# Kernel optimization log

Hardware: AMD Instinct MI355X
Metric: run time of the kernel (lower is better)

Reference implementation:

```python
import jax, jax.numpy as jnp
import numpy as np

N, C, T, H, W = 2, 512, 8, 28, 28
THW = T * H * W
BN_EPS = 1e-5


def conv1x1(x, Wt, b):
    # pointwise channel mixing, equivalent to 1x1 Conv2d/Conv3d on (N,C,T,H,W)
    return jnp.einsum('oc,ncthw->nothw', Wt, x) + b[None, :, None, None, None]


def setup_inputs() -> dict:
    key = jax.random.key(0)
    ks = jax.random.split(key, 8)
    s = 1.0 / np.sqrt(C)
    x = jax.random.normal(ks[0], (N, C, T, H, W), dtype=jnp.float32)
    mask = jax.random.uniform(ks[1], (N, C, T, H, W), dtype=jnp.float32)
    Wh = jax.random.normal(ks[2], (C, C), dtype=jnp.float32) * s
    Wg = jax.random.normal(ks[3], (C, C), dtype=jnp.float32) * s
    Wm = jax.random.normal(ks[4], (C, C), dtype=jnp.float32) * s
    Wz = jax.random.normal(ks[5], (C, C), dtype=jnp.float32) * s  # kaiming-like
    bh = jnp.zeros((C,), jnp.float32)
    bg = jnp.zeros((C,), jnp.float32)
    bm = jnp.zeros((C,), jnp.float32)
    bz = jnp.zeros((C,), jnp.float32)
    bn_w = jnp.ones((C,), jnp.float32)
    bn_b = jnp.zeros((C,), jnp.float32)
    gamma = jnp.float32(1.0)  # self.gamma (undefined in source __init__); learnable scalar
    return dict(x=x, mask=mask, Wh=Wh, bh=bh, Wg=Wg, bg=bg, Wm=Wm, bm=bm,
                Wz=Wz, bz=bz, bn_w=bn_w, bn_b=bn_b, gamma=gamma)


def reference(x, mask, Wh, bh, Wg, bg, Wm, bm, Wz, bz, bn_w, bn_b, gamma):
    n = x.shape[0]
    # proj_f = h(x) reshaped (N, THW, C); proj_g = g(x) (N, C, THW)
    ph_x = conv1x1(x, Wh, bh).reshape(n, C, THW)
    pg = conv1x1(x, Wg, bg).reshape(n, C, THW)
    # energy[n,t,s] = sum_c ph_x[n,c,t] * pg[n,c,s]  -> (N, THW, THW)
    energy = jnp.einsum('nct,ncs->nts', ph_x, pg)
    attention = jax.nn.softmax(energy, axis=-1)
    # proj_h uses self.h on mask (faithful to source)
    ph_m = conv1x1(mask, Wh, bh).reshape(n, C, THW)
    # bmm(proj_h, attention^T): [n,c,t] = sum_s ph_m[n,c,s] * attention[n,t,s]
    mask_energy = jnp.einsum('ncs,nts->nct', ph_m, attention)
    mask_atten = jax.nn.softmax(mask_energy, axis=-1)  # softmax over THW
    pm = conv1x1(x, Wm, bm)
    out = pm * mask_atten.reshape(n, C, T, H, W)
    # W_z: 1x1 Conv3d + BatchNorm3d (training-mode batch stats, weight=1, bias=0)
    wy = conv1x1(x, Wz, bz)
    mu = jnp.mean(wy, axis=(0, 2, 3, 4), keepdims=True)
    var = jnp.var(wy, axis=(0, 2, 3, 4), keepdims=True)
    wy = (wy - mu) * jax.lax.rsqrt(var + BN_EPS)
    wy = wy * bn_w[None, :, None, None, None] + bn_b[None, :, None, None, None]
    return gamma * out + wy
```

## Files before the change

kernel.cpp:

```cpp
#include <hip/hip_runtime.h>
#include <hip/hip_bf16.h>
#include <math.h>

#define NN 2
#define CC 512
#define PP 6272
#define TCHMAX 1664
#define NCHK 4
#define NJT 49
#define KSP 4
#define EM 64.0f
static const size_t PPC = (size_t)PP * CC;
static const size_t NCP = (size_t)NN * PPC;

typedef unsigned short ushortT;
typedef __attribute__((ext_vector_type(8))) short short8;
typedef __attribute__((ext_vector_type(4))) float f32x4;

__device__ __forceinline__ ushortT f2bf(float f) {
  __hip_bfloat16 h = __float2bfloat16(f);
  return *reinterpret_cast<ushortT*>(&h);
}
__device__ __forceinline__ float bf2f(ushortT u) {
  return __uint_as_float(((unsigned)u) << 16);
}

__device__ __forceinline__ void ld_g2l(const void* g, void* l) {
  __builtin_amdgcn_global_load_lds(
      (const __attribute__((address_space(1))) void*)g,
      (__attribute__((address_space(3))) void*)l, 16, 0, 0);
}

__global__ __launch_bounds__(256) void k_cast4(const float* __restrict__ W0,
                                               const float* __restrict__ W1,
                                               const float* __restrict__ W2,
                                               const float* __restrict__ W3,
                                               ushortT* __restrict__ dst) {
  const float* src = (blockIdx.y == 0) ? W0 : (blockIdx.y == 1) ? W1
                    : (blockIdx.y == 2) ? W2 : W3;
  const int i = (blockIdx.x * 256 + threadIdx.x) * 4;
  float4 v = *(const float4*)&src[i];
  ushort4 o;
  o.x = f2bf(v.x); o.y = f2bf(v.y); o.z = f2bf(v.z); o.w = f2bf(v.w);
  *(ushort4*)&dst[(size_t)blockIdx.y * CC * CC + i] = o;
}

__global__ void k_castT(const float* __restrict__ in, ushortT* __restrict__ out) {
  __shared__ float T[32][33];
  const int p0 = blockIdx.x * 32, c0 = blockIdx.y * 32;
  const int tx = threadIdx.x, ty = threadIdx.y;
  const size_t nbi = (size_t)blockIdx.z * PPC;
#pragma unroll
  for (int i = 0; i < 4; ++i)
    T[ty + i * 8][tx] = in[nbi + (size_t)(c0 + ty + i * 8) * PP + p0 + tx];
  __syncthreads();
#pragma unroll
  for (int i = 0; i < 4; ++i) {
    int r = ty + i * 8;
    out[nbi + (size_t)(p0 + r) * CC + c0 + tx] = f2bf(T[tx][r]);
  }
}

template <int OM>
__global__ __launch_bounds__(256) void k_bgemm(const ushortT* __restrict__ A,
                                               const ushortT* __restrict__ B,
                                               const float* __restrict__ bias,
                                               ushortT* __restrict__ out,
                                               int KD, size_t sAn, size_t sBn,
                                               size_t sOn, int ldo) {
  __shared__ __align__(16) ushortT smem[17408];
  ushortT* At = smem;
  ushortT* Bt = smem + 8192;
  const int tid = threadIdx.x;
  const int l = tid & 63, w = tid >> 6;
  const int j0 = blockIdx.x * 128;
  const int i0 = blockIdx.y * 128;
  A += (size_t)blockIdx.z * sAn;
  B += (size_t)blockIdx.z * sBn;
  out += (size_t)blockIdx.z * sOn;
  const int wi = (w & 1) * 64, wj = (w >> 1) * 64;
  const int lr = l & 15, lk = l >> 4;
  const int sr = l >> 3, scg = l & 7;

  f32x4 acc[4][4] = {};

  for (int k0 = 0; k0 < KD; k0 += 64) {
#pragma unroll
    for (int i = 0; i < 4; ++i) {
      int row = w * 32 + i * 8 + sr;
      int cs = scg ^ (row & 7);
      ld_g2l(A + (size_t)(i0 + row) * KD + k0 + cs * 8, (char*)At + (w * 4 + i) * 1024);
      ld_g2l(B + (size_t)(j0 + row) * KD + k0 + cs * 8, (char*)Bt + (w * 4 + i) * 1024);
    }
    __syncthreads();
#pragma unroll
    for (int ks = 0; ks < 2; ++ks) {
      short8 af[4], bfv[4];
      const int cc = ks * 4 + lk;
#pragma unroll
      for (int tt = 0; tt < 4; ++tt) {
        int row = wi + tt * 16 + lr;
        af[tt] = *(const short8*)((const char*)At + row * 128 + ((cc ^ (row & 7)) * 16));
      }
#pragma unroll
      for (int ss = 0; ss < 4; ++ss) {
        int row = wj + ss * 16 + lr;
        bfv[ss] = *(const short8*)((const char*)Bt + row * 128 + ((cc ^ (row & 7)) * 16));
      }
#pragma unroll
      for (int tt = 0; tt < 4; ++tt)
#pragma unroll
        for (int ss = 0; ss < 4; ++ss)
          acc[tt][ss] = __builtin_amdgcn_mfma_f32_16x16x32_bf16(af[tt], bfv[ss], acc[tt][ss], 0, 0, 0);
    }
    __syncthreads();
  }
  const int r4 = (l >> 4) * 4;
  ushortT (*Tr)[136] = (ushortT(*)[136])smem;
  if (OM == 0) {
    float bj[4];
#pragma unroll
    for (int ss = 0; ss < 4; ++ss) bj[ss] = bias[j0 + wj + ss * 16 + lr];
#pragma unroll
    for (int tt = 0; tt < 4; ++tt)
#pragma unroll
      for (int r = 0; r < 4; ++r) {
        int row = wi + tt * 16 + r4 + r;
#pragma unroll
        for (int ss = 0; ss < 4; ++ss)
          Tr[row][wj + ss * 16 + lr] = f2bf(acc[tt][ss][r] + bj[ss]);
      }
  } else {
#pragma unroll
    for (int tt = 0; tt < 4; ++tt)
#pragma unroll
      for (int r = 0; r < 4; ++r) {
        int row = wi + tt * 16 + r4 + r;
        float bi = bias[i0 + row];
#pragma unroll
        for (int ss = 0; ss < 4; ++ss)
          Tr[row][wj + ss * 16 + lr] = f2bf(acc[tt][ss][r] + bi);
      }
  }
  __syncthreads();
#pragma unroll
  for (int q = 0; q < 8; ++q) {
    int chunk = q * 256 + tid;
    int row = chunk >> 4, cg = chunk & 15;
    short8 v = *(const short8*)&Tr[row][cg * 8];
    *(short8*)&out[(size_t)(i0 + row) * ldo + j0 + cg * 8] = v;
  }
}

__global__ __launch_bounds__(256) void k_energy(const ushortT* __restrict__ phxT,
                                                const ushortT* __restrict__ pgT,
                                                ushortT* __restrict__ Ech,
                                                float* __restrict__ Estat,
                                                int tbase) {
  __shared__ __align__(16) ushortT smem[17408];
  __shared__ float Ss[128][2];
  ushortT* At = smem;
  ushortT* Bt = smem + 8192;
  const int tid = threadIdx.x;
  const int l = tid & 63, w = tid >> 6;
  const int j0 = blockIdx.x * 128;
  const int i0 = blockIdx.y * 128;
  const int z = blockIdx.z;
  const ushortT* A = phxT + (size_t)z * PPC + (size_t)tbase * CC;
  const ushortT* B = pgT + (size_t)z * PPC;
  ushortT* out = Ech + (size_t)z * TCHMAX * PP;
  const int wi = (w & 1) * 64, wj = (w >> 1) * 64;
  const int lr = l & 15, lk = l >> 4;
  const int sr = l >> 3, scg = l & 7;

  f32x4 acc[4][4] = {};

  for (int k0 = 0; k0 < CC; k0 += 64) {
#pragma unroll
    for (int i = 0; i < 4; ++i) {
      int row = w * 32 + i * 8 + sr;
      int cs = scg ^ (row & 7);
      ld_g2l(A + (size_t)(i0 + row) * CC + k0 + cs * 8, (char*)At + (w * 4 + i) * 1024);
      ld_g2l(B + (size_t)(j0 + row) * CC + k0 + cs * 8, (char*)Bt + (w * 4 + i) * 1024);
    }
    __syncthreads();
#pragma unroll
    for (int ks = 0; ks < 2; ++ks) {
      short8 af[4], bfv[4];
      const int cc = ks * 4 + lk;
#pragma unroll
      for (int tt = 0; tt < 4; ++tt) {
        int row = wi + tt * 16 + lr;
        af[tt] = *(const short8*)((const char*)At + row * 128 + ((cc ^ (row & 7)) * 16));
      }
#pragma unroll
      for (int ss = 0; ss < 4; ++ss) {
        int row = wj + ss * 16 + lr;
        bfv[ss] = *(const short8*)((const char*)Bt + row * 128 + ((cc ^ (row & 7)) * 16));
      }
#pragma unroll
      for (int tt = 0; tt < 4; ++tt)
#pragma unroll
        for (int ss = 0; ss < 4; ++ss)
          acc[tt][ss] = __builtin_amdgcn_mfma_f32_16x16x32_bf16(af[tt], bfv[ss], acc[tt][ss], 0, 0, 0);
    }
    __syncthreads();
  }
  const int r4 = (l >> 4) * 4;
  const int jh = w >> 1;
  ushortT (*Tr)[136] = (ushortT(*)[136])smem;
#pragma unroll
  for (int tt = 0; tt < 4; ++tt)
#pragma unroll
    for (int r = 0; r < 4; ++r) {
      int row = wi + tt * 16 + r4 + r;
      float u0 = __expf(acc[tt][0][r] - EM);
      float u1 = __expf(acc[tt][1][r] - EM);
      float u2 = __expf(acc[tt][2][r] - EM);
      float u3 = __expf(acc[tt][3][r] - EM);
      Tr[row][wj + lr]      = f2bf(u0);
      Tr[row][wj + 16 + lr] = f2bf(u1);
      Tr[row][wj + 32 + lr] = f2bf(u2);
      Tr[row][wj + 48 + lr] = f2bf(u3);
      float sx = (u0 + u1) + (u2 + u3);
#pragma unroll
      for (int d = 1; d < 16; d <<= 1) sx += __shfl_xor(sx, d);
      if (lr == 0) Ss[row][jh] = sx;
    }
  __syncthreads();
  if (tid < 128) {
    Estat[((size_t)z * TCHMAX + i0 + tid) * NJT + blockIdx.x] =
        Ss[tid][0] + Ss[tid][1];
  }
#pragma unroll
  for (int q = 0; q < 8; ++q) {
    int chunk = q * 256 + tid;
    int row = chunk >> 4, cg = chunk & 15;
    short8 v = *(const short8*)&Tr[row][cg * 8];
    *(short8*)&out[(size_t)(i0 + row) * PP + j0 + cg * 8] = v;
  }
}

__global__ __launch_bounds__(256) void k_zcomb(const float* __restrict__ Estat,
                                               float* __restrict__ rowZ, int rows) {
  const int r = blockIdx.x * 256 + threadIdx.x;
  if (r >= NN * rows) return;
  const int z = r / rows, tl = r % rows;
  const float* p = Estat + ((size_t)z * TCHMAX + tl) * NJT;
  float s = 0.f;
#pragma unroll
  for (int j = 0; j < NJT; ++j) s += p[j];
  rowZ[z * TCHMAX + tl] = 1.0f / s;
}

__global__ __launch_bounds__(256) void k_me(const ushortT* __restrict__ phmB,
                                            const ushortT* __restrict__ Ech,
                                            ushortT* __restrict__ mePart) {
  __shared__ __align__(16) ushortT smem[12288];
  ushortT* At = smem;
  ushortT* Bt = smem + 8192;
  const int tid = threadIdx.x;
  const int l = tid & 63, w = tid >> 6;
  const int tl0 = blockIdx.x * 64;
  const int c0 = blockIdx.y * 128;
  const int bz = blockIdx.z;
  const int z = bz / KSP, ks = bz % KSP;
  const size_t nb = (size_t)z * PPC;
  const ushortT* Pb = Ech + (size_t)z * TCHMAX * PP;
  const int wc = (w & 1) * 64, wt = (w >> 1) * 32;
  const int lr = l & 15, lk = l >> 4;
  const int sr = l >> 3, scg = l & 7;

  f32x4 acc[4][2] = {};

  const int sBeg = ((ks * 98) / KSP) * 64;
  const int sEnd = (((ks + 1) * 98) / KSP) * 64;
  for (int s0 = sBeg; s0 < sEnd; s0 += 64) {
#pragma unroll
    for (int i = 0; i < 4; ++i) {
      int row = w * 32 + i * 8 + sr;
      int cs = scg ^ (row & 7);
      ld_g2l(phmB + nb + (size_t)(c0 + row) * PP + s0 + cs * 8,
             (char*)At + (w * 4 + i) * 1024);
    }
#pragma unroll
    for (int i = 0; i < 2; ++i) {
      int row = w * 16 + i * 8 + sr;
      int cs = scg ^ (row & 7);
      ld_g2l(Pb + (size_t)(tl0 + row) * PP + s0 + cs * 8,
             (char*)Bt + (w * 2 + i) * 1024);
    }
    __syncthreads();
#pragma unroll
    for (int kk = 0; kk < 2; ++kk) {
      short8 af[4], bfv[2];
      const int cc = kk * 4 + lk;
#pragma unroll
      for (int ct = 0; ct < 4; ++ct) {
        int row = wc + ct * 16 + lr;
        af[ct] = *(const short8*)((const char*)At + row * 128 + ((cc ^ (row & 7)) * 16));
      }
#pragma unroll
      for (int tt = 0; tt < 2; ++tt) {
        int row = wt + tt * 16 + lr;
        bfv[tt] = *(const short8*)((const char*)Bt + row * 128 + ((cc ^ (row & 7)) * 16));
      }
#pragma unroll
      for (int ct = 0; ct < 4; ++ct)
#pragma unroll
        for (int tt = 0; tt < 2; ++tt)
          acc[ct][tt] = __builtin_amdgcn_mfma_f32_16x16x32_bf16(af[ct], bfv[tt], acc[ct][tt], 0, 0, 0);
    }
    __syncthreads();
  }
  const int r4 = (l >> 4) * 4;
  ushortT (*Tr)[72] = (ushortT(*)[72])smem;
#pragma unroll
  for (int ct = 0; ct < 4; ++ct)
#pragma unroll
    for (int r = 0; r < 4; ++r) {
      int row = wc + ct * 16 + r4 + r;
#pragma unroll
      for (int tt = 0; tt < 2; ++tt)
        Tr[row][wt + tt * 16 + lr] = f2bf(acc[ct][tt][r]);
    }
  __syncthreads();
  ushortT* out = mePart + ((size_t)(ks * NN + z) * CC) * TCHMAX;
#pragma unroll
  for (int q = 0; q < 4; ++q) {
    int chunk = q * 256 + tid;
    int row = chunk >> 3, cg = chunk & 7;
    short8 v = *(const short8*)&Tr[row][cg * 8];
    *(short8*)&out[(size_t)(c0 + row) * TCHMAX + tl0 + cg * 8] = v;
  }
}

__global__ __launch_bounds__(256) void k_meadd(const ushortT* __restrict__ mePart,
                                               const float* __restrict__ rowZ,
                                               ushortT* __restrict__ meb,
                                               int tbase, int rows) {
  const int idx = (blockIdx.x * 256 + threadIdx.x) * 4;
  const int tl = idx % rows;
  const int c = (idx / rows) % CC;
  const int z = idx / (rows * CC);
  float s0 = 0.f, s1 = 0.f, s2 = 0.f, s3 = 0.f;
#pragma unroll
  for (int ks = 0; ks < KSP; ++ks) {
    const size_t o = ((size_t)(ks * NN + z) * CC + c) * TCHMAX + tl;
    ushort4 a = *(const ushort4*)&mePart[o];
    s0 += bf2f(a.x); s1 += bf2f(a.y); s2 += bf2f(a.z); s3 += bf2f(a.w);
  }
  const float4 rz = *(const float4*)&rowZ[z * TCHMAX + tl];
  ushort4 v;
  v.x = f2bf(s0 * rz.x); v.y = f2bf(s1 * rz.y);
  v.z = f2bf(s2 * rz.z); v.w = f2bf(s3 * rz.w);
  *(ushort4*)&meb[((size_t)z * CC + c) * PP + tbase + tl] = v;
}

__global__ __launch_bounds__(256) void k_soft2(const ushortT* __restrict__ me,
                                               float* __restrict__ m2,
                                               float* __restrict__ Z2) {
  __shared__ float red[256];
  const ushortT* row = me + (size_t)blockIdx.x * PP;
  const int tid = threadIdx.x;
  const int NCH = PP / 8;
  float m = -INFINITY;
  for (int i = tid; i < NCH; i += 256) {
    short8 v = *(const short8*)&row[i * 8];
#pragma unroll
    for (int j = 0; j < 8; ++j) m = fmaxf(m, bf2f((ushortT)v[j]));
  }
  red[tid] = m;
  __syncthreads();
  for (int s = 128; s > 0; s >>= 1) {
    if (tid < s) red[tid] = fmaxf(red[tid], red[tid + s]);
    __syncthreads();
  }
  m = red[0];
  __syncthreads();
  float zz = 0.f;
  for (int i = tid; i < NCH; i += 256) {
    short8 v = *(const short8*)&row[i * 8];
#pragma unroll
    for (int j = 0; j < 8; ++j) zz += __expf(bf2f((ushortT)v[j]) - m);
  }
  red[tid] = zz;
  __syncthreads();
  for (int s = 128; s > 0; s >>= 1) {
    if (tid < s) red[tid] += red[tid + s];
    __syncthreads();
  }
  if (tid == 0) { m2[blockIdx.x] = m; Z2[blockIdx.x] = red[0]; }
}

__global__ __launch_bounds__(256) void k_bnstat(const ushortT* __restrict__ wz,
                                                float* __restrict__ mu,
                                                float* __restrict__ rinv) {
  __shared__ float rs[256];
  __shared__ float rq[256];
  const int c = blockIdx.x;
  const int tid = threadIdx.x;
  const int NCH = PP / 8;
  float s = 0.f, q = 0.f;
  for (int n = 0; n < NN; ++n) {
    const ushortT* rowp = wz + (size_t)n * CC * PP + (size_t)c * PP;
    for (int i = tid; i < NCH; i += 256) {
      short8 v = *(const short8*)&rowp[i * 8];
#pragma unroll
      for (int j = 0; j < 8; ++j) {
        float f = bf2f((ushortT)v[j]);
        s += f;
        q += f * f;
      }
    }
  }
  rs[tid] = s; rq[tid] = q;
  __syncthreads();
  for (int st = 128; st > 0; st >>= 1) {
    if (tid < st) { rs[tid] += rs[tid + st]; rq[tid] += rq[tid + st]; }
    __syncthreads();
  }
  if (tid == 0) {
    const float inv_n = 1.0f / (float)(NN * PP);
    float mean = rs[0] * inv_n;
    float var = rq[0] * inv_n - mean * mean;
    mu[c] = mean;
    rinv[c] = rsqrtf(var + 1e-5f);
  }
}

__global__ __launch_bounds__(256) void k_final(const ushortT* __restrict__ pmB,
                                               const ushortT* __restrict__ me,
                                               const ushortT* __restrict__ wz,
                                               const float* __restrict__ m2,
                                               const float* __restrict__ Z2,
                                               const float* __restrict__ mu,
                                               const float* __restrict__ rinv,
                                               const float* __restrict__ bnw,
                                               const float* __restrict__ bnb,
                                               const float* __restrict__ gamma,
                                               float* __restrict__ out) {
  const int e4 = blockIdx.x * 256 + threadIdx.x;
  const size_t e = (size_t)e4 * 4;
  const int nc = (int)(e / PP);
  const int c = nc & (CC - 1);
  const float m = m2[nc];
  const float rz = 1.0f / Z2[nc];
  const float mub = mu[c];
  const float ri = rinv[c] * bnw[c];
  const float bb = bnb[c];
  const float g = gamma[0];
  ushort4 pv = *(const ushort4*)&pmB[e];
  ushort4 mev = *(const ushort4*)&me[e];
  ushort4 wzv = *(const ushort4*)&wz[e];
  float4 o;
  o.x = g * bf2f(pv.x) * (__expf(bf2f(mev.x) - m) * rz) + (bf2f(wzv.x) - mub) * ri + bb;
  o.y = g * bf2f(pv.y) * (__expf(bf2f(mev.y) - m) * rz) + (bf2f(wzv.y) - mub) * ri + bb;
  o.z = g * bf2f(pv.z) * (__expf(bf2f(mev.z) - m) * rz) + (bf2f(wzv.z) - mub) * ri + bb;
  o.w = g * bf2f(pv.w) * (__expf(bf2f(mev.w) - m) * rz) + (bf2f(wzv.w) - mub) * ri + bb;
  *(float4*)&out[e] = o;
}

extern "C" void kernel_launch(void* const* d_in, const int* in_sizes, int n_in,
                              void* d_out, int out_size, void* d_ws, size_t ws_size,
                              hipStream_t stream) {
  (void)in_sizes; (void)n_in; (void)out_size; (void)ws_size;
  const float* x    = (const float*)d_in[0];
  const float* mask = (const float*)d_in[1];
  const float* Wh   = (const float*)d_in[2];
  const float* bh   = (const float*)d_in[3];
  const float* Wg   = (const float*)d_in[4];
  const float* bg   = (const float*)d_in[5];
  const float* Wm   = (const float*)d_in[6];
  const float* bm   = (const float*)d_in[7];
  const float* Wz   = (const float*)d_in[8];
  const float* bz   = (const float*)d_in[9];
  const float* bnw  = (const float*)d_in[10];
  const float* bnb  = (const float*)d_in[11];
  const float* gam  = (const float*)d_in[12];

  ushortT* wzb  = (ushortT*)d_ws;
  ushortT* meb  = wzb + NCP;
  ushortT* pmB  = meb + NCP;
  ushortT* phxT = pmB + NCP;
  ushortT* pgT  = phxT + NCP;
  ushortT* phmB = pgT + NCP;
  ushortT* Wbf  = phmB + NCP;
  ushortT* Whbf = Wbf;
  ushortT* Wgbf = Wbf + 1 * CC * CC;
  ushortT* Wmbf = Wbf + 2 * CC * CC;
  ushortT* Wzbf = Wbf + 3 * CC * CC;
  float* m2    = (float*)(Wbf + 4 * CC * CC);
  float* Z2    = m2 + NN * CC;
  float* mu    = Z2 + NN * CC;
  float* rin   = mu + CC;
  float* Estat = rin + CC;
  float* rowZ  = Estat + (size_t)NN * TCHMAX * NJT;
  float* region = rowZ + (size_t)NN * TCHMAX + 16;
  ushortT* xT    = (ushortT*)region;
  ushortT* maskT = xT + NCP;
  ushortT* Ech    = (ushortT*)region;
  ushortT* mePart = Ech + (size_t)NN * TCHMAX * PP;

  k_cast4<<<dim3(256, 4), 256, 0, stream>>>(Wh, Wg, Wm, Wz, Wbf);
  dim3 gct(PP / 32, CC / 32, NN);
  k_castT<<<gct, dim3(32, 8), 0, stream>>>(x, xT);
  k_castT<<<gct, dim3(32, 8), 0, stream>>>(mask, maskT);

  dim3 gPc(CC / 128, PP / 128, NN);
  k_bgemm<0><<<gPc, 256, 0, stream>>>(xT, Whbf, bh, phxT, CC, PPC, 0, PPC, CC);
  k_bgemm<0><<<gPc, 256, 0, stream>>>(xT, Wgbf, bg, pgT, CC, PPC, 0, PPC, CC);
  dim3 gCp(PP / 128, CC / 128, NN);
  k_bgemm<1><<<gCp, 256, 0, stream>>>(Whbf, maskT, bh, phmB, CC, 0, PPC, PPC, PP);
  k_bgemm<1><<<gCp, 256, 0, stream>>>(Wmbf, xT, bm, pmB, CC, 0, PPC, PPC, PP);
  k_bgemm<1><<<gCp, 256, 0, stream>>>(Wzbf, xT, bz, wzb, CC, 0, PPC, PPC, PP);

  static const int chunkTiles[NCHK] = {13, 12, 12, 12};
  int tbase = 0;
  for (int ch = 0; ch < NCHK; ++ch) {
    const int tiles = chunkTiles[ch];
    const int rows = tiles * 128;
    dim3 gE(NJT, tiles, NN);
    k_energy<<<gE, 256, 0, stream>>>(phxT, pgT, Ech, Estat, tbase);
    k_zcomb<<<(NN * rows + 255) / 256, 256, 0, stream>>>(Estat, rowZ, rows);
    dim3 gM(rows / 64, CC / 128, NN * KSP);
    k_me<<<gM, 256, 0, stream>>>(phmB, Ech, mePart);
    k_meadd<<<NN * CC * rows / 1024, 256, 0, stream>>>(mePart, rowZ, meb, tbase, rows);
    tbase += rows;
  }

  k_soft2<<<NN * CC, 256, 0, stream>>>(meb, m2, Z2);
  k_bnstat<<<CC, 256, 0, stream>>>(wzb, mu, rin);
  const int total4 = (int)(NCP / 4);
  k_final<<<total4 / 256, 256, 0, stream>>>(pmB, meb, wzb, m2, Z2, mu, rin,
                                            bnw, bnb, gam, (float*)d_out);
}
```

Measured before the change: 595.6 us.

## Fuse projection GEMMs, remap workgroups across XCDs, raise split-K, drop LDS epilogues

The five separate 1x1-conv GEMMs become one k_convs launch that shares the staged x tile between paired projections (h/g and m/z), and the two transpose casts merge into one launch. The energy and mask-energy kernels remap workgroup IDs so neighbouring tiles land on the same XCD for L2 reuse. They also write results straight from registers in transposed fragment order instead of staging through LDS. Split-K for the mask-energy GEMM rises from 4 to 8 when the workspace is large enough. The changes cut launch count, redundant operand loads and epilogue LDS traffic, at the cost of more registers in the fused GEMM and narrower uncoalesced ushort4 stores.

```diff
diff --git a/kernel.cpp b/kernel.cpp
--- a/kernel.cpp
+++ b/kernel.cpp
@@ -8,7 +8,6 @@
 #define TCHMAX 1664
 #define NCHK 4
 #define NJT 49
-#define KSP 4
 #define EM 64.0f
 static const size_t PPC = (size_t)PP * CC;
 static const size_t NCP = (size_t)NN * PPC;
@@ -29,6 +28,12 @@
   __builtin_amdgcn_global_load_lds(
       (const __attribute__((address_space(1))) void*)g,
       (__attribute__((address_space(3))) void*)l, 16, 0, 0);
+}
+
+__device__ __forceinline__ int xcd_remap(int orig, int nwg) {
+  const int q = nwg >> 3, r = nwg & 7;
+  const int x = orig & 7, lo = orig >> 3;
+  return (x < r) ? x * (q + 1) + lo : r * (q + 1) + (x - r) * q + lo;
 }
 
 __global__ __launch_bounds__(256) void k_cast4(const float* __restrict__ W0,
@@ -45,11 +50,17 @@
   *(ushort4*)&dst[(size_t)blockIdx.y * CC * CC + i] = o;
 }
 
-__global__ void k_castT(const float* __restrict__ in, ushortT* __restrict__ out) {
+__global__ void k_castT2(const float* __restrict__ x,
+                         const float* __restrict__ mask,
+                         ushortT* __restrict__ xT,
+                         ushortT* __restrict__ maskT) {
   __shared__ float T[32][33];
+  const int zz = blockIdx.z;
+  const float* in = (zz < 2) ? x : mask;
+  ushortT* out = (zz < 2) ? xT : maskT;
   const int p0 = blockIdx.x * 32, c0 = blockIdx.y * 32;
   const int tx = threadIdx.x, ty = threadIdx.y;
-  const size_t nbi = (size_t)blockIdx.z * PPC;
+  const size_t nbi = (size_t)(zz & 1) * PPC;
 #pragma unroll
   for (int i = 0; i < 4; ++i)
     T[ty + i * 8][tx] = in[nbi + (size_t)(c0 + ty + i * 8) * PP + p0 + tx];
@@ -61,94 +72,189 @@
   }
 }
 
-template <int OM>
-__global__ __launch_bounds__(256) void k_bgemm(const ushortT* __restrict__ A,
-                                               const ushortT* __restrict__ B,
-                                               const float* __restrict__ bias,
-                                               ushortT* __restrict__ out,
-                                               int KD, size_t sAn, size_t sBn,
-                                               size_t sOn, int ldo) {
-  __shared__ __align__(16) ushortT smem[17408];
-  ushortT* At = smem;
-  ushortT* Bt = smem + 8192;
+__global__ __launch_bounds__(256) void k_convs(
+    const ushortT* __restrict__ xT, const ushortT* __restrict__ maskT,
+    const ushortT* __restrict__ Whbf, const ushortT* __restrict__ Wgbf,
+    const ushortT* __restrict__ Wmbf, const ushortT* __restrict__ Wzbf,
+    const float* __restrict__ bh, const float* __restrict__ bg,
+    const float* __restrict__ bm, const float* __restrict__ bz,
+    ushortT* __restrict__ phxT, ushortT* __restrict__ pgT,
+    ushortT* __restrict__ phmB, ushortT* __restrict__ pmB,
+    ushortT* __restrict__ wzb) {
+  __shared__ __align__(16) ushortT smem[24576];
+  ushortT* S0 = smem;
+  ushortT* S1 = smem + 8192;
+  ushortT* S2 = smem + 16384;
   const int tid = threadIdx.x;
   const int l = tid & 63, w = tid >> 6;
-  const int j0 = blockIdx.x * 128;
-  const int i0 = blockIdx.y * 128;
-  A += (size_t)blockIdx.z * sAn;
-  B += (size_t)blockIdx.z * sBn;
-  out += (size_t)blockIdx.z * sOn;
-  const int wi = (w & 1) * 64, wj = (w >> 1) * 64;
+  const int orig = blockIdx.x;
+  const int wgid = (orig & 7) * 147 + (orig >> 3);
+  const int zq = wgid / 196;
+  const int within = wgid % 196;
+  const int ctile = within & 3;
+  const int ptile = within >> 2;
+  const int wA = (w & 1) * 64, wB = (w >> 1) * 64;
   const int lr = l & 15, lk = l >> 4;
   const int sr = l >> 3, scg = l & 7;
-
-  f32x4 acc[4][4] = {};
-
-  for (int k0 = 0; k0 < KD; k0 += 64) {
+  const int r4 = (l >> 4) * 4;
+
+  auto stage = [&](const ushortT* src, int baseRow, ushortT* dst, int k0) {
 #pragma unroll
     for (int i = 0; i < 4; ++i) {
       int row = w * 32 + i * 8 + sr;
       int cs = scg ^ (row & 7);
-      ld_g2l(A + (size_t)(i0 + row) * KD + k0 + cs * 8, (char*)At + (w * 4 + i) * 1024);
-      ld_g2l(B + (size_t)(j0 + row) * KD + k0 + cs * 8, (char*)Bt + (w * 4 + i) * 1024);
-    }
-    __syncthreads();
-#pragma unroll
-    for (int ks = 0; ks < 2; ++ks) {
-      short8 af[4], bfv[4];
-      const int cc = ks * 4 + lk;
-#pragma unroll
-      for (int tt = 0; tt < 4; ++tt) {
-        int row = wi + tt * 16 + lr;
-        af[tt] = *(const short8*)((const char*)At + row * 128 + ((cc ^ (row & 7)) * 16));
-      }
+      ld_g2l(src + (size_t)(baseRow + row) * CC + k0 + cs * 8,
+             (char*)dst + (w * 4 + i) * 1024);
+    }
+  };
+  auto ldf = [&](const ushortT* base, int rbase, int cc_, short8* f) {
+#pragma unroll
+    for (int t = 0; t < 4; ++t) {
+      int row = rbase + t * 16 + lr;
+      f[t] = *(const short8*)((const char*)base + row * 128 +
+                              ((cc_ ^ (row & 7)) * 16));
+    }
+  };
+
+  if (zq < 2) {
+    const int zb = zq;
+    const ushortT* A = xT + (size_t)zb * PPC;
+    ushortT* o1 = phxT + (size_t)zb * PPC;
+    ushortT* o2 = pgT + (size_t)zb * PPC;
+    const int p0 = ptile * 128, c0 = ctile * 128;
+    f32x4 a1[4][4] = {}, a2[4][4] = {};
+    for (int k0 = 0; k0 < CC; k0 += 64) {
+      stage(A, p0, S0, k0);
+      stage(Whbf, c0, S1, k0);
+      stage(Wgbf, c0, S2, k0);
+      __syncthreads();
+#pragma unroll
+      for (int ks = 0; ks < 2; ++ks) {
+        short8 fp[4], f1[4], f2[4];
+        const int cc = ks * 4 + lk;
+        ldf(S0, wA, cc, fp);
+        ldf(S1, wB, cc, f1);
+        ldf(S2, wB, cc, f2);
+#pragma unroll
+        for (int ss = 0; ss < 4; ++ss)
+#pragma unroll
+          for (int tt = 0; tt < 4; ++tt) {
+            a1[ss][tt] = __builtin_amdgcn_mfma_f32_16x16x32_bf16(f1[ss], fp[tt], a1[ss][tt], 0, 0, 0);
+            a2[ss][tt] = __builtin_amdgcn_mfma_f32_16x16x32_bf16(f2[ss], fp[tt], a2[ss][tt], 0, 0, 0);
+          }
+      }
+      __syncthreads();
+    }
+#pragma unroll
+    for (int tt = 0; tt < 4; ++tt) {
+      const size_t prow = (size_t)(p0 + wA + tt * 16 + lr) * CC;
 #pragma unroll
       for (int ss = 0; ss < 4; ++ss) {
-        int row = wj + ss * 16 + lr;
-        bfv[ss] = *(const short8*)((const char*)Bt + row * 128 + ((cc ^ (row & 7)) * 16));
-      }
-#pragma unroll
-      for (int tt = 0; tt < 4; ++tt)
+        const int co = c0 + wB + ss * 16 + r4;
+        float4 b1v = *(const float4*)&bh[co];
+        float4 b2v = *(const float4*)&bg[co];
+        ushort4 v1, v2;
+        v1.x = f2bf(a1[ss][tt][0] + b1v.x);
+        v1.y = f2bf(a1[ss][tt][1] + b1v.y);
+        v1.z = f2bf(a1[ss][tt][2] + b1v.z);
+        v1.w = f2bf(a1[ss][tt][3] + b1v.w);
+        v2.x = f2bf(a2[ss][tt][0] + b2v.x);
+        v2.y = f2bf(a2[ss][tt][1] + b2v.y);
+        v2.z = f2bf(a2[ss][tt][2] + b2v.z);
+        v2.w = f2bf(a2[ss][tt][3] + b2v.w);
+        *(ushort4*)&o1[prow + co] = v1;
+        *(ushort4*)&o2[prow + co] = v2;
+      }
+    }
+  } else if (zq < 4) {
+    const int zb = zq - 2;
+    const ushortT* B = maskT + (size_t)zb * PPC;
+    ushortT* o = phmB + (size_t)zb * PPC;
+    const int s0 = ptile * 128, c0 = ctile * 128;
+    f32x4 a[4][4] = {};
+    for (int k0 = 0; k0 < CC; k0 += 64) {
+      stage(Whbf, c0, S0, k0);
+      stage(B, s0, S1, k0);
+      __syncthreads();
+#pragma unroll
+      for (int ks = 0; ks < 2; ++ks) {
+        short8 fs[4], fc[4];
+        const int cc = ks * 4 + lk;
+        ldf(S1, wA, cc, fs);
+        ldf(S0, wB, cc, fc);
 #pragma unroll
         for (int ss = 0; ss < 4; ++ss)
-          acc[tt][ss] = __builtin_amdgcn_mfma_f32_16x16x32_bf16(af[tt], bfv[ss], acc[tt][ss], 0, 0, 0);
-    }
-    __syncthreads();
-  }
-  const int r4 = (l >> 4) * 4;
-  ushortT (*Tr)[136] = (ushortT(*)[136])smem;
-  if (OM == 0) {
-    float bj[4];
-#pragma unroll
-    for (int ss = 0; ss < 4; ++ss) bj[ss] = bias[j0 + wj + ss * 16 + lr];
-#pragma unroll
-    for (int tt = 0; tt < 4; ++tt)
-#pragma unroll
-      for (int r = 0; r < 4; ++r) {
-        int row = wi + tt * 16 + r4 + r;
+#pragma unroll
+          for (int tt = 0; tt < 4; ++tt)
+            a[ss][tt] = __builtin_amdgcn_mfma_f32_16x16x32_bf16(fs[ss], fc[tt], a[ss][tt], 0, 0, 0);
+      }
+      __syncthreads();
+    }
+#pragma unroll
+    for (int tt = 0; tt < 4; ++tt) {
+      const int c = c0 + wB + tt * 16 + lr;
+      const float bi = bh[c];
+      const size_t crow = (size_t)c * PP;
+#pragma unroll
+      for (int ss = 0; ss < 4; ++ss) {
+        ushort4 v;
+        v.x = f2bf(a[ss][tt][0] + bi);
+        v.y = f2bf(a[ss][tt][1] + bi);
+        v.z = f2bf(a[ss][tt][2] + bi);
+        v.w = f2bf(a[ss][tt][3] + bi);
+        *(ushort4*)&o[crow + s0 + wA + ss * 16 + r4] = v;
+      }
+    }
+  } else {
+    const int zb = zq - 4;
+    const ushortT* B = xT + (size_t)zb * PPC;
+    ushortT* o1 = pmB + (size_t)zb * PPC;
+    ushortT* o2 = wzb + (size_t)zb * PPC;
+    const int p0 = ptile * 128, c0 = ctile * 128;
+    f32x4 a1[4][4] = {}, a2[4][4] = {};
+    for (int k0 = 0; k0 < CC; k0 += 64) {
+      stage(Wmbf, c0, S0, k0);
+      stage(Wzbf, c0, S1, k0);
+      stage(B, p0, S2, k0);
+      __syncthreads();
+#pragma unroll
+      for (int ks = 0; ks < 2; ++ks) {
+        short8 fx[4], fm[4], fz[4];
+        const int cc = ks * 4 + lk;
+        ldf(S2, wA, cc, fx);
+        ldf(S0, wB, cc, fm);
+        ldf(S1, wB, cc, fz);
 #pragma unroll
         for (int ss = 0; ss < 4; ++ss)
-          Tr[row][wj + ss * 16 + lr] = f2bf(acc[tt][ss][r] + bj[ss]);
-      }
-  } else {
-#pragma unroll
-    for (int tt = 0; tt < 4; ++tt)
-#pragma unroll
-      for (int r = 0; r < 4; ++r) {
-        int row = wi + tt * 16 + r4 + r;
-        float bi = bias[i0 + row];
-#pragma unroll
-        for (int ss = 0; ss < 4; ++ss)
-          Tr[row][wj + ss * 16 + lr] = f2bf(acc[tt][ss][r] + bi);
-      }
-  }
-  __syncthreads();
-#pragma unroll
-  for (int q = 0; q < 8; ++q) {
-    int chunk = q * 256 + tid;
-    int row = chunk >> 4, cg = chunk & 15;
-    short8 v = *(const short8*)&Tr[row][cg * 8];
-    *(short8*)&out[(size_t)(i0 + row) * ldo + j0 + cg * 8] = v;
+#pragma unroll
+          for (int tt = 0; tt < 4; ++tt) {
+            a1[ss][tt] = __builtin_amdgcn_mfma_f32_16x16x32_bf16(fx[ss], fm[tt], a1[ss][tt], 0, 0, 0);
+            a2[ss][tt] = __builtin_amdgcn_mfma_f32_16x16x32_bf16(fx[ss], fz[tt], a2[ss][tt], 0, 0, 0);
+          }
+      }
+      __syncthreads();
+    }
+#pragma unroll
+    for (int tt = 0; tt < 4; ++tt) {
+      const int c = c0 + wB + tt * 16 + lr;
+      const float b1v = bm[c], b2v = bz[c];
+      const size_t crow = (size_t)c * PP;
+#pragma unroll
+      for (int ss = 0; ss < 4; ++ss) {
+        const size_t off = crow + p0 + wA + ss * 16 + r4;
+        ushort4 v1, v2;
+        v1.x = f2bf(a1[ss][tt][0] + b1v);
+        v1.y = f2bf(a1[ss][tt][1] + b1v);
+        v1.z = f2bf(a1[ss][tt][2] + b1v);
+        v1.w = f2bf(a1[ss][tt][3] + b1v);
+        v2.x = f2bf(a2[ss][tt][0] + b2v);
+        v2.y = f2bf(a2[ss][tt][1] + b2v);
+        v2.z = f2bf(a2[ss][tt][2] + b2v);
+        v2.w = f2bf(a2[ss][tt][3] + b2v);
+        *(ushort4*)&o1[off] = v1;
+        *(ushort4*)&o2[off] = v2;
+      }
+    }
   }
 }
 
@@ -157,21 +263,27 @@
                                                 ushortT* __restrict__ Ech,
                                                 float* __restrict__ Estat,
                                                 int tbase) {
-  __shared__ __align__(16) ushortT smem[17408];
+  __shared__ __align__(16) ushortT smem[16384];
   __shared__ float Ss[128][2];
   ushortT* At = smem;
   ushortT* Bt = smem + 8192;
   const int tid = threadIdx.x;
   const int l = tid & 63, w = tid >> 6;
-  const int j0 = blockIdx.x * 128;
-  const int i0 = blockIdx.y * 128;
-  const int z = blockIdx.z;
+  const int tiles = gridDim.y;
+  const int orig = blockIdx.x + NJT * (blockIdx.y + tiles * blockIdx.z);
+  const int wgid = xcd_remap(orig, NJT * tiles * NN);
+  const int it = wgid % tiles;
+  const int jt = (wgid / tiles) % NJT;
+  const int z = wgid / (tiles * NJT);
+  const int j0 = jt * 128;
+  const int i0 = it * 128;
   const ushortT* A = phxT + (size_t)z * PPC + (size_t)tbase * CC;
   const ushortT* B = pgT + (size_t)z * PPC;
   ushortT* out = Ech + (size_t)z * TCHMAX * PP;
   const int wi = (w & 1) * 64, wj = (w >> 1) * 64;
   const int lr = l & 15, lk = l >> 4;
   const int sr = l >> 3, scg = l & 7;
+  const int r4 = (l >> 4) * 4;
 
   f32x4 acc[4][4] = {};
 
@@ -199,45 +311,36 @@
         bfv[ss] = *(const short8*)((const char*)Bt + row * 128 + ((cc ^ (row & 7)) * 16));
       }
 #pragma unroll
-      for (int tt = 0; tt < 4; ++tt)
-#pragma unroll
-        for (int ss = 0; ss < 4; ++ss)
-          acc[tt][ss] = __builtin_amdgcn_mfma_f32_16x16x32_bf16(af[tt], bfv[ss], acc[tt][ss], 0, 0, 0);
+      for (int ss = 0; ss < 4; ++ss)
+#pragma unroll
+        for (int tt = 0; tt < 4; ++tt)
+          acc[ss][tt] = __builtin_amdgcn_mfma_f32_16x16x32_bf16(bfv[ss], af[tt], acc[ss][tt], 0, 0, 0);
     }
     __syncthreads();
   }
-  const int r4 = (l >> 4) * 4;
-  const int jh = w >> 1;
-  ushortT (*Tr)[136] = (ushortT(*)[136])smem;
-#pragma unroll
-  for (int tt = 0; tt < 4; ++tt)
-#pragma unroll
-    for (int r = 0; r < 4; ++r) {
-      int row = wi + tt * 16 + r4 + r;
-      float u0 = __expf(acc[tt][0][r] - EM);
-      float u1 = __expf(acc[tt][1][r] - EM);
-      float u2 = __expf(acc[tt][2][r] - EM);
-      float u3 = __expf(acc[tt][3][r] - EM);
-      Tr[row][wj + lr]      = f2bf(u0);
-      Tr[row][wj + 16 + lr] = f2bf(u1);
-      Tr[row][wj + 32 + lr] = f2bf(u2);
-      Tr[row][wj + 48 + lr] = f2bf(u3);
-      float sx = (u0 + u1) + (u2 + u3);
-#pragma unroll
-      for (int d = 1; d < 16; d <<= 1) sx += __shfl_xor(sx, d);
-      if (lr == 0) Ss[row][jh] = sx;
-    }
+#pragma unroll
+  for (int tt = 0; tt < 4; ++tt) {
+    const int trow = i0 + wi + tt * 16 + lr;
+    ushortT* orow = out + (size_t)trow * PP + j0;
+    float sx = 0.f;
+#pragma unroll
+    for (int ss = 0; ss < 4; ++ss) {
+      float u0 = __expf(acc[ss][tt][0] - EM);
+      float u1 = __expf(acc[ss][tt][1] - EM);
+      float u2 = __expf(acc[ss][tt][2] - EM);
+      float u3 = __expf(acc[ss][tt][3] - EM);
+      sx += (u0 + u1) + (u2 + u3);
+      ushort4 v;
+      v.x = f2bf(u0); v.y = f2bf(u1); v.z = f2bf(u2); v.w = f2bf(u3);
+      *(ushort4*)&orow[wj + ss * 16 + r4] = v;
+    }
+    sx += __shfl_xor(sx, 16);
+    sx += __shfl_xor(sx, 32);
+    if (l < 16) Ss[wi + tt * 16 + l][w >> 1] = sx;
+  }
   __syncthreads();
   if (tid < 128) {
-    Estat[((size_t)z * TCHMAX + i0 + tid) * NJT + blockIdx.x] =
-        Ss[tid][0] + Ss[tid][1];
-  }
-#pragma unroll
-  for (int q = 0; q < 8; ++q) {
-    int chunk = q * 256 + tid;
-    int row = chunk >> 4, cg = chunk & 15;
-    short8 v = *(const short8*)&Tr[row][cg * 8];
-    *(short8*)&out[(size_t)(i0 + row) * PP + j0 + cg * 8] = v;
+    Estat[((size_t)z * TCHMAX + i0 + tid) * NJT + jt] = Ss[tid][0] + Ss[tid][1];
   }
 }
 
@@ -253,6 +356,7 @@
   rowZ[z * TCHMAX + tl] = 1.0f / s;
 }
 
+template <int KSPT>
 __global__ __launch_bounds__(256) void k_me(const ushortT* __restrict__ phmB,
                                             const ushortT* __restrict__ Ech,
                                             ushortT* __restrict__ mePart) {
@@ -261,20 +365,27 @@
   ushortT* Bt = smem + 8192;
   const int tid = threadIdx.x;
   const int l = tid & 63, w = tid >> 6;
-  const int tl0 = blockIdx.x * 64;
-  const int c0 = blockIdx.y * 128;
-  const int bz = blockIdx.z;
-  const int z = bz / KSP, ks = bz % KSP;
+  const int gx = gridDim.x;
+  const int orig = blockIdx.x + gx * (blockIdx.y + 4 * blockIdx.z);
+  const int nwg = gx * 4 * (NN * KSPT);
+  const int wgid = (orig & 7) * (nwg >> 3) + (orig >> 3);
+  const int cb = wgid & 3;
+  const int tl = (wgid >> 2) % gx;
+  const int bz = (wgid >> 2) / gx;
+  const int tl0 = tl * 64;
+  const int c0 = cb * 128;
+  const int z = bz / KSPT, ks = bz % KSPT;
   const size_t nb = (size_t)z * PPC;
   const ushortT* Pb = Ech + (size_t)z * TCHMAX * PP;
   const int wc = (w & 1) * 64, wt = (w >> 1) * 32;
   const int lr = l & 15, lk = l >> 4;
   const int sr = l >> 3, scg = l & 7;
-
-  f32x4 acc[4][2] = {};
-
-  const int sBeg = ((ks * 98) / KSP) * 64;
-  const int sEnd = (((ks + 1) * 98) / KSP) * 64;
+  const int r4 = (l >> 4) * 4;
+
+  f32x4 acc[2][4] = {};
+
+  const int sBeg = ((ks * 98) / KSPT) * 64;
+  const int sEnd = (((ks + 1) * 98) / KSPT) * 64;
   for (int s0 = sBeg; s0 < sEnd; s0 += 64) {
 #pragma unroll
     for (int i = 0; i < 4; ++i) {
@@ -306,35 +417,30 @@
         bfv[tt] = *(const short8*)((const char*)Bt + row * 128 + ((cc ^ (row & 7)) * 16));
       }
 #pragma unroll
-      for (int ct = 0; ct < 4; ++ct)
-#pragma unroll
-        for (int tt = 0; tt < 2; ++tt)
-          acc[ct][tt] = __builtin_amdgcn_mfma_f32_16x16x32_bf16(af[ct], bfv[tt], acc[ct][tt], 0, 0, 0);
+      for (int tt = 0; tt < 2; ++tt)
+#pragma unroll
+        for (int ct = 0; ct < 4; ++ct)
+          acc[tt][ct] = __builtin_amdgcn_mfma_f32_16x16x32_bf16(bfv[tt], af[ct], acc[tt][ct], 0, 0, 0);
     }
     __syncthreads();
   }
-  const int r4 = (l >> 4) * 4;
-  ushortT (*Tr)[72] = (ushortT(*)[72])smem;
-#pragma unroll
-  for (int ct = 0; ct < 4; ++ct)
-#pragma unroll
-    for (int r = 0; r < 4; ++r) {
-      int row = wc + ct * 16 + r4 + r;
-#pragma unroll
-      for (int tt = 0; tt < 2; ++tt)
-        Tr[row][wt + tt * 16 + lr] = f2bf(acc[ct][tt][r]);
-    }
-  __syncthreads();
   ushortT* out = mePart + ((size_t)(ks * NN + z) * CC) * TCHMAX;
 #pragma unroll
-  for (int q = 0; q < 4; ++q) {
-    int chunk = q * 256 + tid;
-    int row = chunk >> 3, cg = chunk & 7;
-    short8 v = *(const short8*)&Tr[row][cg * 8];
-    *(short8*)&out[(size_t)(c0 + row) * TCHMAX + tl0 + cg * 8] = v;
-  }
-}
-
+  for (int ct = 0; ct < 4; ++ct) {
+    const size_t crow = (size_t)(c0 + wc + ct * 16 + lr) * TCHMAX + tl0;
+#pragma unroll
+    for (int tt = 0; tt < 2; ++tt) {
+      ushort4 v;
+      v.x = f2bf(acc[tt][ct][0]);
+      v.y = f2bf(acc[tt][ct][1]);
+      v.z = f2bf(acc[tt][ct][2]);
+      v.w = f2bf(acc[tt][ct][3]);
+      *(ushort4*)&out[crow + wt + tt * 16 + r4] = v;
+    }
+  }
+}
+
+template <int KSPT>
 __global__ __launch_bounds__(256) void k_meadd(const ushortT* __restrict__ mePart,
                                                const float* __restrict__ rowZ,
                                                ushortT* __restrict__ meb,
@@ -345,7 +451,7 @@
   const int z = idx / (rows * CC);
   float s0 = 0.f, s1 = 0.f, s2 = 0.f, s3 = 0.f;
 #pragma unroll
-  for (int ks = 0; ks < KSP; ++ks) {
+  for (int ks = 0; ks < KSPT; ++ks) {
     const size_t o = ((size_t)(ks * NN + z) * CC + c) * TCHMAX + tl;
     ushort4 a = *(const ushort4*)&mePart[o];
     s0 += bf2f(a.x); s1 += bf2f(a.y); s2 += bf2f(a.z); s3 += bf2f(a.w);
@@ -464,7 +570,7 @@
 extern "C" void kernel_launch(void* const* d_in, const int* in_sizes, int n_in,
                               void* d_out, int out_size, void* d_ws, size_t ws_size,
                               hipStream_t stream) {
-  (void)in_sizes; (void)n_in; (void)out_size; (void)ws_size;
+  (void)in_sizes; (void)n_in; (void)out_size;
   const float* x    = (const float*)d_in[0];
   const float* mask = (const float*)d_in[1];
   const float* Wh   = (const float*)d_in[2];
@@ -502,18 +608,16 @@
   ushortT* Ech    = (ushortT*)region;
   ushortT* mePart = Ech + (size_t)NN * TCHMAX * PP;
 
+  const size_t regionOffB = (size_t)((char*)region - (char*)d_ws);
+  const size_t need8 = regionOffB +
+      ((size_t)NN * TCHMAX * PP + 8ull * NN * CC * TCHMAX) * 2;
+  const bool k8 = ws_size >= need8;
+
   k_cast4<<<dim3(256, 4), 256, 0, stream>>>(Wh, Wg, Wm, Wz, Wbf);
-  dim3 gct(PP / 32, CC / 32, NN);
-  k_castT<<<gct, dim3(32, 8), 0, stream>>>(x, xT);
-  k_castT<<<gct, dim3(32, 8), 0, stream>>>(mask, maskT);
-
-  dim3 gPc(CC / 128, PP / 128, NN);
-  k_bgemm<0><<<gPc, 256, 0, stream>>>(xT, Whbf, bh, phxT, CC, PPC, 0, PPC, CC);
-  k_bgemm<0><<<gPc, 256, 0, stream>>>(xT, Wgbf, bg, pgT, CC, PPC, 0, PPC, CC);
-  dim3 gCp(PP / 128, CC / 128, NN);
-  k_bgemm<1><<<gCp, 256, 0, stream>>>(Whbf, maskT, bh, phmB, CC, 0, PPC, PPC, PP);
-  k_bgemm<1><<<gCp, 256, 0, stream>>>(Wmbf, xT, bm, pmB, CC, 0, PPC, PPC, PP);
-  k_bgemm<1><<<gCp, 256, 0, stream>>>(Wzbf, xT, bz, wzb, CC, 0, PPC, PPC, PP);
+  k_castT2<<<dim3(PP / 32, CC / 32, 4), dim3(32, 8), 0, stream>>>(x, mask, xT, maskT);
+
+  k_convs<<<1176, 256, 0, stream>>>(xT, maskT, Whbf, Wgbf, Wmbf, Wzbf,
+                                    bh, bg, bm, bz, phxT, pgT, phmB, pmB, wzb);
 
   static const int chunkTiles[NCHK] = {13, 12, 12, 12};
   int tbase = 0;
@@ -523,9 +627,17 @@
     dim3 gE(NJT, tiles, NN);
     k_energy<<<gE, 256, 0, stream>>>(phxT, pgT, Ech, Estat, tbase);
     k_zcomb<<<(NN * rows + 255) / 256, 256, 0, stream>>>(Estat, rowZ, rows);
-    dim3 gM(rows / 64, CC / 128, NN * KSP);
-    k_me<<<gM, 256, 0, stream>>>(phmB, Ech, mePart);
-    k_meadd<<<NN * CC * rows / 1024, 256, 0, stream>>>(mePart, rowZ, meb, tbase, rows);
+    if (k8) {
+      dim3 gM(rows / 64, CC / 128, NN * 8);
+      k_me<8><<<gM, 256, 0, stream>>>(phmB, Ech, mePart);
+      k_meadd<8><<<NN * CC * rows / 1024, 256, 0, stream>>>(mePart, rowZ, meb,
+                                                            tbase, rows);
+    } else {
+      dim3 gM(rows / 64, CC / 128, NN * 4);
+      k_me<4><<<gM, 256, 0, stream>>>(phmB, Ech, mePart);
+      k_meadd<4><<<NN * CC * rows / 1024, 256, 0, stream>>>(mePart, rowZ, meb,
+                                                            tbase, rows);
+    }
     tbase += rows;
   }
 
```

After: 561.2 us. -5.8%, faster.
